# Kernel optimization log

Measured on AMD Instinct MI355X. Metric: run time of the kernel, lower is better.

The kernel has to match this reference:

```python
import jax, jax.numpy as jnp
import numpy as np

DIM = 1024
NUM_HEADS = 16
HEAD_DIM = DIM // NUM_HEADS
SCALE = HEAD_DIM ** -0.5


def setup_inputs() -> dict:
    key = jax.random.key(0)
    k_x, k_wqkv, k_bqkv, k_wp, k_bp = jax.random.split(key, 5)
    B, C, D = 4, 1024, DIM
    x = jax.random.normal(k_x, (B, C, D), dtype=jnp.float32)
    # nn.Linear stores weight as (out, in); we keep (in, out) for x @ W
    w_qkv = jax.random.normal(k_wqkv, (D, 3 * D), dtype=jnp.float32) * (D ** -0.5)
    b_qkv = jax.random.normal(k_bqkv, (3 * D,), dtype=jnp.float32) * 0.02
    w_proj = jax.random.normal(k_wp, (D, D), dtype=jnp.float32) * (D ** -0.5)
    b_proj = jax.random.normal(k_bp, (D,), dtype=jnp.float32) * 0.02
    return {"x": x, "w_qkv": w_qkv, "b_qkv": b_qkv, "w_proj": w_proj, "b_proj": b_proj}


def reference(x, w_qkv, b_qkv, w_proj, b_proj):
    B, C, D = x.shape
    H, Hd = NUM_HEADS, HEAD_DIM
    qkv = x @ w_qkv + b_qkv                       # (B, C, 3D)
    qkv = qkv.reshape(B, C, 3, H, Hd)
    q = qkv[:, :, 0].transpose(0, 2, 1, 3)        # (B, H, C, Hd)
    k = qkv[:, :, 1].transpose(0, 2, 1, 3)
    v = qkv[:, :, 2].transpose(0, 2, 1, 3)
    attn = jnp.einsum('bhqd,bhkd->bhqk', q, k) * SCALE
    attn = jax.nn.softmax(attn, axis=-1)
    out = jnp.einsum('bhqk,bhkd->bhqd', attn, v)  # (B, H, C, Hd)
    out = out.transpose(0, 2, 1, 3).reshape(B, C, D)
    return out @ w_proj + b_proj
```

## Files before the change

kernel.cpp:

```cpp
#include <hip/hip_runtime.h>
#include <cstdint>

#define BB 4
#define CC 1024
#define DD 1024
#define HH 16
#define HD 64
#define NH3 3072

typedef __attribute__((ext_vector_type(8))) short short8;
typedef __attribute__((ext_vector_type(4))) float f32x4;

#define MFMA16(a, b, c) __builtin_amdgcn_mfma_f32_16x16x32_bf16(a, b, c, 0, 0, 0)

__device__ __forceinline__ void glds16(const void* g, void* l) {
    __builtin_amdgcn_global_load_lds(
        (const __attribute__((address_space(1))) void*)g,
        (__attribute__((address_space(3))) void*)l, 16, 0, 0);
}

__device__ __forceinline__ ushort f2bf(float f) {
    union { float f; uint32_t u; } v; v.f = f;
    uint32_t r = v.u + 0x7FFF + ((v.u >> 16) & 1);
    return (ushort)(r >> 16);
}

__device__ __forceinline__ uint32_t pack2bf(float a, float b) {
    return (uint32_t)f2bf(a) | ((uint32_t)f2bf(b) << 16);
}

__global__ __launch_bounds__(256)
void convert_f32_bf16(const float* __restrict__ in, ushort* __restrict__ out, int n4)
{
    int i = blockIdx.x * 256 + threadIdx.x;
    if (i < n4) {
        float4 v = ((const float4*)in)[i];
        ushort4 o;
        o.x = f2bf(v.x); o.y = f2bf(v.y); o.z = f2bf(v.z); o.w = f2bf(v.w);
        ((ushort4*)out)[i] = o;
    }
}

__global__ __launch_bounds__(256)
void transpose_w(const float* __restrict__ in, ushort* __restrict__ out, int K, int N)
{
    __shared__ float Ts[64 * 65];
    const int n0 = blockIdx.x * 64, k0 = blockIdx.y * 64;
    const int t = threadIdx.x;
    #pragma unroll
    for (int i = 0; i < 16; ++i) {
        int idx = t + i * 256;
        int r = idx >> 6, c = idx & 63;
        Ts[r * 65 + c] = in[(size_t)(k0 + r) * N + n0 + c];
    }
    __syncthreads();
    #pragma unroll
    for (int i = 0; i < 16; ++i) {
        int idx = t + i * 256;
        int rr = idx >> 6, cc = idx & 63;
        out[(size_t)(n0 + rr) * K + k0 + cc] = f2bf(Ts[cc * 65 + rr]);
    }
}

__global__ __launch_bounds__(256)
void vtrans(const ushort* __restrict__ vb, ushort* __restrict__ vt)
{
    __shared__ ushort Ts[64 * 66];
    const int ct = blockIdx.x, bh = blockIdx.y;
    const ushort* src = vb + ((size_t)bh * CC + ct * 64) * HD;
    ushort* dst = vt + (size_t)bh * HD * CC + ct * 64;
    const int t = threadIdx.x;
    #pragma unroll
    for (int i = 0; i < 16; ++i) {
        int idx = t + i * 256;
        int r = idx >> 6, c = idx & 63;
        Ts[r * 66 + c] = src[r * 64 + c];
    }
    __syncthreads();
    #pragma unroll
    for (int i = 0; i < 16; ++i) {
        int idx = t + i * 256;
        int hd = idx >> 6, c = idx & 63;
        dst[(size_t)hd * CC + c] = Ts[c * 66 + hd];
    }
}

template<int MODE>
__global__ __launch_bounds__(256)
void gemm_bt(const ushort* __restrict__ A, const ushort* __restrict__ Bt,
             const float* __restrict__ bias, float* __restrict__ Cf,
             ushort* __restrict__ qb, ushort* __restrict__ kb, ushort* __restrict__ vb,
             int M, int N, int K)
{
    __shared__ ushort As[128 * 32];
    __shared__ ushort Bs[128 * 32];

    const int tid = threadIdx.x;
    const int wid = tid >> 6, lane = tid & 63;
    const int quad = lane >> 4, l15 = lane & 15;
    const int m0 = blockIdx.y * 128, n0 = blockIdx.x * 128;
    const int wm = (wid >> 1) * 64, wn = (wid & 1) * 64;

    const int sr = lane >> 2;
    const int sc = lane & 3;

    f32x4 acc[4][4];
    #pragma unroll
    for (int i = 0; i < 4; ++i)
        #pragma unroll
        for (int j = 0; j < 4; ++j) acc[i][j] = (f32x4)(0.0f);

    for (int k0 = 0; k0 < K; k0 += 32) {
        __syncthreads();
        #pragma unroll
        for (int t = 0; t < 2; ++t) {
            int r = wid * 32 + t * 16 + sr;
            int cg = sc ^ ((r >> 1) & 3);
            glds16(A  + (size_t)(m0 + r) * K + k0 + cg * 8, As + (wid * 32 + t * 16) * 32);
            glds16(Bt + (size_t)(n0 + r) * K + k0 + cg * 8, Bs + (wid * 32 + t * 16) * 32);
        }
        __syncthreads();

        short8 af[4], bf[4];
        #pragma unroll
        for (int i = 0; i < 4; ++i) {
            int row = wm + i * 16 + l15;
            af[i] = *(const short8*)(As + row * 32 + (quad ^ ((row >> 1) & 3)) * 8);
            int col = wn + i * 16 + l15;
            bf[i] = *(const short8*)(Bs + col * 32 + (quad ^ ((col >> 1) & 3)) * 8);
        }
        #pragma unroll
        for (int i = 0; i < 4; ++i)
            #pragma unroll
            for (int j = 0; j < 4; ++j)
                acc[i][j] = MFMA16(af[i], bf[j], acc[i][j]);
    }

    if (MODE == 0) {
        #pragma unroll
        for (int i = 0; i < 4; ++i) {
            int row = m0 + wm + i * 16 + quad * 4;
            #pragma unroll
            for (int j = 0; j < 4; ++j) {
                int col = n0 + wn + j * 16 + l15;
                float bv = bias[col];
                #pragma unroll
                for (int r = 0; r < 4; ++r)
                    Cf[(size_t)(row + r) * N + col] = acc[i][j][r] + bv;
            }
        }
    } else {
        #pragma unroll
        for (int j = 0; j < 4; ++j) {
            int n = n0 + wn + j * 16 + l15;
            int three = n >> 10;
            int h = (n >> 6) & 15;
            int hd = n & 63;
            ushort* base = (three == 0) ? qb : ((three == 1) ? kb : vb);
            float scale = (three == 0) ? 0.1803368801f : 1.0f;
            float bv = bias[n];
            #pragma unroll
            for (int i = 0; i < 4; ++i) {
                int row = m0 + wm + i * 16 + quad * 4;
                #pragma unroll
                for (int r = 0; r < 4; ++r) {
                    int m = row + r;
                    int b = m >> 10, c = m & 1023;
                    base[((size_t)((b * HH + h) * CC) + c) * HD + hd] =
                        f2bf((acc[i][j][r] + bv) * scale);
                }
            }
        }
    }
}

__global__ __launch_bounds__(256)
void attn_mfma2(const ushort* __restrict__ qb, const ushort* __restrict__ kb,
                const ushort* __restrict__ vt, ushort* __restrict__ attnb)
{
    __shared__ ushort Qs[128 * 64];
    __shared__ ushort Ks[64 * 64];
    __shared__ ushort Vs[64 * 64];
    __shared__ ushort Ps[128 * 72];

    const int tid = threadIdx.x;
    const int wid = tid >> 6, lane = tid & 63;
    const int quad = lane >> 4, l15 = lane & 15;
    const int qt = blockIdx.x, bh = blockIdx.y;
    const int q0 = qt * 128;
    const int b = bh >> 4, h = bh & 15;

    const ushort* Qp  = qb + ((size_t)bh * CC + q0) * HD;
    const ushort* Kp  = kb + (size_t)bh * CC * HD;
    const ushort* Vtp = vt + (size_t)bh * HD * CC;

    const int sr = lane >> 3;
    const int sc = lane & 7;

    #pragma unroll
    for (int t = 0; t < 4; ++t) {
        int r = wid * 32 + t * 8 + sr;
        int cg = sc ^ (r & 7);
        glds16(Qp + (size_t)r * HD + cg * 8, Qs + (wid * 32 + t * 8) * 64);
    }
    __syncthreads();

    short8 qf[2][2];
    #pragma unroll
    for (int q2 = 0; q2 < 2; ++q2) {
        int row = wid * 32 + q2 * 16 + l15;
        #pragma unroll
        for (int s = 0; s < 2; ++s)
            qf[q2][s] = *(const short8*)(Qs + row * 64 + (((s * 4 + quad) ^ (row & 7)) * 8));
    }

    f32x4 oacc[2][4];
    #pragma unroll
    for (int q2 = 0; q2 < 2; ++q2)
        #pragma unroll
        for (int hb = 0; hb < 4; ++hb) oacc[q2][hb] = (f32x4)(0.0f);
    float lsum[2] = {0.0f, 0.0f};

    for (int kt = 0; kt < 16; ++kt) {
        __syncthreads();
        #pragma unroll
        for (int t = 0; t < 2; ++t) {
            int r = wid * 16 + t * 8 + sr;
            int cg = sc ^ (r & 7);
            glds16(Kp  + ((size_t)(kt * 64 + r)) * HD + cg * 8, Ks + (wid * 16 + t * 8) * 64);
            glds16(Vtp + (size_t)r * CC + kt * 64 + cg * 8,     Vs + (wid * 16 + t * 8) * 64);
        }
        __syncthreads();

        #pragma unroll
        for (int kb2 = 0; kb2 < 4; ++kb2) {
            int krow = kb2 * 16 + l15;
            short8 kf0 = *(const short8*)(Ks + krow * 64 + ((quad ^ (krow & 7)) * 8));
            short8 kf1 = *(const short8*)(Ks + krow * 64 + (((4 + quad) ^ (krow & 7)) * 8));
            #pragma unroll
            for (int q2 = 0; q2 < 2; ++q2) {
                f32x4 st = (f32x4)(0.0f);
                st = MFMA16(kf0, qf[q2][0], st);
                st = MFMA16(kf1, qf[q2][1], st);
                float p0 = exp2f(st[0]);
                float p1 = exp2f(st[1]);
                float p2 = exp2f(st[2]);
                float p3 = exp2f(st[3]);
                lsum[q2] += (p0 + p1) + (p2 + p3);
                int row = wid * 32 + q2 * 16 + l15;
                *(uint2*)(Ps + row * 72 + kb2 * 16 + quad * 4) =
                    make_uint2(pack2bf(p0, p1), pack2bf(p2, p3));
            }
        }

        short8 vf[4][2];
        #pragma unroll
        for (int hb = 0; hb < 4; ++hb) {
            int hr = hb * 16 + l15;
            vf[hb][0] = *(const short8*)(Vs + hr * 64 + ((quad ^ (hr & 7)) * 8));
            vf[hb][1] = *(const short8*)(Vs + hr * 64 + (((4 + quad) ^ (hr & 7)) * 8));
        }
        #pragma unroll
        for (int q2 = 0; q2 < 2; ++q2) {
            int row = wid * 32 + q2 * 16 + l15;
            short8 pf0 = *(const short8*)(Ps + row * 72 + quad * 8);
            short8 pf1 = *(const short8*)(Ps + row * 72 + 32 + quad * 8);
            #pragma unroll
            for (int hb = 0; hb < 4; ++hb) {
                oacc[q2][hb] = MFMA16(pf0, vf[hb][0], oacc[q2][hb]);
                oacc[q2][hb] = MFMA16(pf1, vf[hb][1], oacc[q2][hb]);
            }
        }
    }

    #pragma unroll
    for (int q2 = 0; q2 < 2; ++q2) {
        lsum[q2] += __shfl_xor(lsum[q2], 16);
        lsum[q2] += __shfl_xor(lsum[q2], 32);
    }

    #pragma unroll
    for (int q2 = 0; q2 < 2; ++q2) {
        #pragma unroll
        for (int r = 0; r < 4; ++r) {
            float inv = 1.0f / __shfl(lsum[q2], (lane & 48) | (quad * 4 + r));
            int c = q0 + wid * 32 + q2 * 16 + quad * 4 + r;
            #pragma unroll
            for (int hb = 0; hb < 4; ++hb) {
                int d = h * 64 + hb * 16 + l15;
                attnb[((size_t)(b * CC + c)) * DD + d] = f2bf(oacc[q2][hb][r] * inv);
            }
        }
    }
}

extern "C" void kernel_launch(void* const* d_in, const int* in_sizes, int n_in,
                              void* d_out, int out_size, void* d_ws, size_t ws_size,
                              hipStream_t stream)
{
    (void)in_sizes; (void)n_in; (void)out_size; (void)ws_size;
    const float* x      = (const float*)d_in[0];
    const float* w_qkv  = (const float*)d_in[1];
    const float* b_qkv  = (const float*)d_in[2];
    const float* w_proj = (const float*)d_in[3];
    const float* b_proj = (const float*)d_in[4];
    float* out = (float*)d_out;

    ushort* p = (ushort*)d_ws;
    ushort* xbf   = p;  p += (size_t)4 * 1024 * 1024;
    ushort* wqkvT = p;  p += (size_t)3 * 1024 * 1024;
    ushort* wprjT = p;  p += (size_t)1 * 1024 * 1024;
    ushort* qbuf  = p;  p += (size_t)4 * 1024 * 1024;
    ushort* kbuf  = p;  p += (size_t)4 * 1024 * 1024;
    ushort* vbuf  = p;  p += (size_t)4 * 1024 * 1024;
    ushort* vtb   = p;  p += (size_t)4 * 1024 * 1024;
    ushort* attnb = p;  p += (size_t)4 * 1024 * 1024;

    convert_f32_bf16<<<4096, 256, 0, stream>>>(x, xbf, 1024 * 1024);
    transpose_w<<<dim3(48, 16), 256, 0, stream>>>(w_qkv, wqkvT, DD, NH3);
    transpose_w<<<dim3(16, 16), 256, 0, stream>>>(w_proj, wprjT, DD, DD);

    gemm_bt<1><<<dim3(NH3 / 128, (BB * CC) / 128), 256, 0, stream>>>(
        xbf, wqkvT, b_qkv, nullptr, qbuf, kbuf, vbuf, BB * CC, NH3, DD);

    vtrans<<<dim3(16, 64), 256, 0, stream>>>(vbuf, vtb);

    attn_mfma2<<<dim3(8, 64), 256, 0, stream>>>(qbuf, kbuf, vtb, attnb);

    gemm_bt<0><<<dim3(DD / 128, (BB * CC) / 128), 256, 0, stream>>>(
        attnb, wprjT, b_proj, out, nullptr, nullptr, nullptr, BB * CC, DD, DD);
}
```

Baseline: 208.0 us.

## Double-buffer GEMM and attention tiles, fuse prep kernels, write V transposed

```diff
diff --git a/kernel.cpp b/kernel.cpp
--- a/kernel.cpp
+++ b/kernel.cpp
@@ -30,23 +30,33 @@
 }
 
 __global__ __launch_bounds__(256)
-void convert_f32_bf16(const float* __restrict__ in, ushort* __restrict__ out, int n4)
+void prep_kernel(const float* __restrict__ x, ushort* __restrict__ xbf,
+                 const float* __restrict__ wqkv, ushort* __restrict__ wqkvT,
+                 const float* __restrict__ wprj, ushort* __restrict__ wprjT)
 {
-    int i = blockIdx.x * 256 + threadIdx.x;
-    if (i < n4) {
-        float4 v = ((const float4*)in)[i];
+    __shared__ float Ts[64 * 65];
+    const int blk = blockIdx.x;
+    const int t = threadIdx.x;
+
+    if (blk < 4096) {
+        int i = blk * 256 + t;
+        float4 v = ((const float4*)x)[i];
         ushort4 o;
         o.x = f2bf(v.x); o.y = f2bf(v.y); o.z = f2bf(v.z); o.w = f2bf(v.w);
-        ((ushort4*)out)[i] = o;
-    }
-}
-
-__global__ __launch_bounds__(256)
-void transpose_w(const float* __restrict__ in, ushort* __restrict__ out, int K, int N)
-{
-    __shared__ float Ts[64 * 65];
-    const int n0 = blockIdx.x * 64, k0 = blockIdx.y * 64;
-    const int t = threadIdx.x;
+        ((ushort4*)xbf)[i] = o;
+        return;
+    }
+
+    const float* in; ushort* outp; int K, N, n0, k0;
+    if (blk < 4864) {
+        int bx = blk - 4096;
+        in = wqkv; outp = wqkvT; K = DD; N = NH3;
+        n0 = (bx % 48) * 64; k0 = (bx / 48) * 64;
+    } else {
+        int bx = blk - 4864;
+        in = wprj; outp = wprjT; K = DD; N = DD;
+        n0 = (bx % 16) * 64; k0 = (bx / 16) * 64;
+    }
     #pragma unroll
     for (int i = 0; i < 16; ++i) {
         int idx = t + i * 256;
@@ -58,30 +68,7 @@
     for (int i = 0; i < 16; ++i) {
         int idx = t + i * 256;
         int rr = idx >> 6, cc = idx & 63;
-        out[(size_t)(n0 + rr) * K + k0 + cc] = f2bf(Ts[cc * 65 + rr]);
-    }
-}
-
-__global__ __launch_bounds__(256)
-void vtrans(const ushort* __restrict__ vb, ushort* __restrict__ vt)
-{
-    __shared__ ushort Ts[64 * 66];
-    const int ct = blockIdx.x, bh = blockIdx.y;
-    const ushort* src = vb + ((size_t)bh * CC + ct * 64) * HD;
-    ushort* dst = vt + (size_t)bh * HD * CC + ct * 64;
-    const int t = threadIdx.x;
-    #pragma unroll
-    for (int i = 0; i < 16; ++i) {
-        int idx = t + i * 256;
-        int r = idx >> 6, c = idx & 63;
-        Ts[r * 66 + c] = src[r * 64 + c];
-    }
-    __syncthreads();
-    #pragma unroll
-    for (int i = 0; i < 16; ++i) {
-        int idx = t + i * 256;
-        int hd = idx >> 6, c = idx & 63;
-        dst[(size_t)hd * CC + c] = Ts[c * 66 + hd];
+        outp[(size_t)(n0 + rr) * K + k0 + cc] = f2bf(Ts[cc * 65 + rr]);
     }
 }
 
@@ -89,11 +76,11 @@
 __global__ __launch_bounds__(256)
 void gemm_bt(const ushort* __restrict__ A, const ushort* __restrict__ Bt,
              const float* __restrict__ bias, float* __restrict__ Cf,
-             ushort* __restrict__ qb, ushort* __restrict__ kb, ushort* __restrict__ vb,
+             ushort* __restrict__ qb, ushort* __restrict__ kb, ushort* __restrict__ vtb,
              int M, int N, int K)
 {
-    __shared__ ushort As[128 * 32];
-    __shared__ ushort Bs[128 * 32];
+    __shared__ ushort As[2][128 * 32];
+    __shared__ ushort Bs[2][128 * 32];
 
     const int tid = threadIdx.x;
     const int wid = tid >> 6, lane = tid & 63;
@@ -104,36 +91,52 @@
     const int sr = lane >> 2;
     const int sc = lane & 3;
 
+    const int r0 = wid * 32 + sr;
+    const int cg0 = sc ^ ((r0 >> 1) & 3);
+    const int cg1 = sc ^ (((r0 + 16) >> 1) & 3);
+    const ushort* Ar0 = A  + (size_t)(m0 + r0) * K + cg0 * 8;
+    const ushort* Ar1 = A  + (size_t)(m0 + r0 + 16) * K + cg1 * 8;
+    const ushort* Br0 = Bt + (size_t)(n0 + r0) * K + cg0 * 8;
+    const ushort* Br1 = Bt + (size_t)(n0 + r0 + 16) * K + cg1 * 8;
+
     f32x4 acc[4][4];
     #pragma unroll
     for (int i = 0; i < 4; ++i)
         #pragma unroll
         for (int j = 0; j < 4; ++j) acc[i][j] = (f32x4)(0.0f);
 
+    {
+        glds16(Ar0, &As[0][(wid * 32) * 32]);
+        glds16(Br0, &Bs[0][(wid * 32) * 32]);
+        glds16(Ar1, &As[0][(wid * 32 + 16) * 32]);
+        glds16(Br1, &Bs[0][(wid * 32 + 16) * 32]);
+    }
+
+    int buf = 0;
     for (int k0 = 0; k0 < K; k0 += 32) {
         __syncthreads();
-        #pragma unroll
-        for (int t = 0; t < 2; ++t) {
-            int r = wid * 32 + t * 16 + sr;
-            int cg = sc ^ ((r >> 1) & 3);
-            glds16(A  + (size_t)(m0 + r) * K + k0 + cg * 8, As + (wid * 32 + t * 16) * 32);
-            glds16(Bt + (size_t)(n0 + r) * K + k0 + cg * 8, Bs + (wid * 32 + t * 16) * 32);
-        }
-        __syncthreads();
+        if (k0 + 32 < K) {
+            const int kn = k0 + 32;
+            glds16(Ar0 + kn, &As[buf ^ 1][(wid * 32) * 32]);
+            glds16(Br0 + kn, &Bs[buf ^ 1][(wid * 32) * 32]);
+            glds16(Ar1 + kn, &As[buf ^ 1][(wid * 32 + 16) * 32]);
+            glds16(Br1 + kn, &Bs[buf ^ 1][(wid * 32 + 16) * 32]);
+        }
 
         short8 af[4], bf[4];
         #pragma unroll
         for (int i = 0; i < 4; ++i) {
             int row = wm + i * 16 + l15;
-            af[i] = *(const short8*)(As + row * 32 + (quad ^ ((row >> 1) & 3)) * 8);
+            af[i] = *(const short8*)(&As[buf][row * 32 + (quad ^ ((row >> 1) & 3)) * 8]);
             int col = wn + i * 16 + l15;
-            bf[i] = *(const short8*)(Bs + col * 32 + (quad ^ ((col >> 1) & 3)) * 8);
+            bf[i] = *(const short8*)(&Bs[buf][col * 32 + (quad ^ ((col >> 1) & 3)) * 8]);
         }
         #pragma unroll
         for (int i = 0; i < 4; ++i)
             #pragma unroll
             for (int j = 0; j < 4; ++j)
                 acc[i][j] = MFMA16(af[i], bf[j], acc[i][j]);
+        buf ^= 1;
     }
 
     if (MODE == 0) {
@@ -156,7 +159,6 @@
             int three = n >> 10;
             int h = (n >> 6) & 15;
             int hd = n & 63;
-            ushort* base = (three == 0) ? qb : ((three == 1) ? kb : vb);
             float scale = (three == 0) ? 0.1803368801f : 1.0f;
             float bv = bias[n];
             #pragma unroll
@@ -166,8 +168,13 @@
                 for (int r = 0; r < 4; ++r) {
                     int m = row + r;
                     int b = m >> 10, c = m & 1023;
-                    base[((size_t)((b * HH + h) * CC) + c) * HD + hd] =
-                        f2bf((acc[i][j][r] + bv) * scale);
+                    ushort val = f2bf((acc[i][j][r] + bv) * scale);
+                    if (three == 0)
+                        qb[((size_t)((b * HH + h) * CC) + c) * HD + hd] = val;
+                    else if (three == 1)
+                        kb[((size_t)((b * HH + h) * CC) + c) * HD + hd] = val;
+                    else
+                        vtb[((size_t)((b * HH + h) * HD) + hd) * CC + c] = val;
                 }
             }
         }
@@ -175,12 +182,11 @@
 }
 
 __global__ __launch_bounds__(256)
-void attn_mfma2(const ushort* __restrict__ qb, const ushort* __restrict__ kb,
+void attn_mfma3(const ushort* __restrict__ qb, const ushort* __restrict__ kb,
                 const ushort* __restrict__ vt, ushort* __restrict__ attnb)
 {
-    __shared__ ushort Qs[128 * 64];
-    __shared__ ushort Ks[64 * 64];
-    __shared__ ushort Vs[64 * 64];
+    __shared__ ushort Ks[2][64 * 64];
+    __shared__ ushort Vs[2][64 * 64];
     __shared__ ushort Ps[128 * 72];
 
     const int tid = threadIdx.x;
@@ -197,22 +203,27 @@
     const int sr = lane >> 3;
     const int sc = lane & 7;
 
-    #pragma unroll
-    for (int t = 0; t < 4; ++t) {
-        int r = wid * 32 + t * 8 + sr;
-        int cg = sc ^ (r & 7);
-        glds16(Qp + (size_t)r * HD + cg * 8, Qs + (wid * 32 + t * 8) * 64);
-    }
-    __syncthreads();
-
     short8 qf[2][2];
     #pragma unroll
     for (int q2 = 0; q2 < 2; ++q2) {
         int row = wid * 32 + q2 * 16 + l15;
         #pragma unroll
         for (int s = 0; s < 2; ++s)
-            qf[q2][s] = *(const short8*)(Qs + row * 64 + (((s * 4 + quad) ^ (row & 7)) * 8));
-    }
+            qf[q2][s] = *(const short8*)(Qp + (size_t)row * HD + (s * 4 + quad) * 8);
+    }
+
+    const int kr = wid * 16 + sr;
+    const int cgA = sc ^ (kr & 7);
+    const int cgB = sc ^ ((kr + 8) & 7);
+    const ushort* Kr0 = Kp  + (size_t)kr * HD + cgA * 8;
+    const ushort* Kr1 = Kp  + (size_t)(kr + 8) * HD + cgB * 8;
+    const ushort* Vr0 = Vtp + (size_t)kr * CC + cgA * 8;
+    const ushort* Vr1 = Vtp + (size_t)(kr + 8) * CC + cgB * 8;
+
+    glds16(Kr0, &Ks[0][(wid * 16) * 64]);
+    glds16(Vr0, &Vs[0][(wid * 16) * 64]);
+    glds16(Kr1, &Ks[0][(wid * 16 + 8) * 64]);
+    glds16(Vr1, &Vs[0][(wid * 16 + 8) * 64]);
 
     f32x4 oacc[2][4];
     #pragma unroll
@@ -221,22 +232,22 @@
         for (int hb = 0; hb < 4; ++hb) oacc[q2][hb] = (f32x4)(0.0f);
     float lsum[2] = {0.0f, 0.0f};
 
+    int buf = 0;
     for (int kt = 0; kt < 16; ++kt) {
         __syncthreads();
-        #pragma unroll
-        for (int t = 0; t < 2; ++t) {
-            int r = wid * 16 + t * 8 + sr;
-            int cg = sc ^ (r & 7);
-            glds16(Kp  + ((size_t)(kt * 64 + r)) * HD + cg * 8, Ks + (wid * 16 + t * 8) * 64);
-            glds16(Vtp + (size_t)r * CC + kt * 64 + cg * 8,     Vs + (wid * 16 + t * 8) * 64);
-        }
-        __syncthreads();
+        if (kt < 15) {
+            const int koff = (kt + 1) * 64;
+            glds16(Kr0 + (size_t)koff * HD, &Ks[buf ^ 1][(wid * 16) * 64]);
+            glds16(Vr0 + koff,              &Vs[buf ^ 1][(wid * 16) * 64]);
+            glds16(Kr1 + (size_t)koff * HD, &Ks[buf ^ 1][(wid * 16 + 8) * 64]);
+            glds16(Vr1 + koff,              &Vs[buf ^ 1][(wid * 16 + 8) * 64]);
+        }
 
         #pragma unroll
         for (int kb2 = 0; kb2 < 4; ++kb2) {
             int krow = kb2 * 16 + l15;
-            short8 kf0 = *(const short8*)(Ks + krow * 64 + ((quad ^ (krow & 7)) * 8));
-            short8 kf1 = *(const short8*)(Ks + krow * 64 + (((4 + quad) ^ (krow & 7)) * 8));
+            short8 kf0 = *(const short8*)(&Ks[buf][krow * 64 + ((quad ^ (krow & 7)) * 8)]);
+            short8 kf1 = *(const short8*)(&Ks[buf][krow * 64 + (((4 + quad) ^ (krow & 7)) * 8)]);
             #pragma unroll
             for (int q2 = 0; q2 < 2; ++q2) {
                 f32x4 st = (f32x4)(0.0f);
@@ -257,8 +268,8 @@
         #pragma unroll
         for (int hb = 0; hb < 4; ++hb) {
             int hr = hb * 16 + l15;
-            vf[hb][0] = *(const short8*)(Vs + hr * 64 + ((quad ^ (hr & 7)) * 8));
-            vf[hb][1] = *(const short8*)(Vs + hr * 64 + (((4 + quad) ^ (hr & 7)) * 8));
+            vf[hb][0] = *(const short8*)(&Vs[buf][hr * 64 + ((quad ^ (hr & 7)) * 8)]);
+            vf[hb][1] = *(const short8*)(&Vs[buf][hr * 64 + (((4 + quad) ^ (hr & 7)) * 8)]);
         }
         #pragma unroll
         for (int q2 = 0; q2 < 2; ++q2) {
@@ -271,6 +282,7 @@
                 oacc[q2][hb] = MFMA16(pf1, vf[hb][1], oacc[q2][hb]);
             }
         }
+        buf ^= 1;
     }
 
     #pragma unroll
@@ -312,20 +324,15 @@
     ushort* wprjT = p;  p += (size_t)1 * 1024 * 1024;
     ushort* qbuf  = p;  p += (size_t)4 * 1024 * 1024;
     ushort* kbuf  = p;  p += (size_t)4 * 1024 * 1024;
-    ushort* vbuf  = p;  p += (size_t)4 * 1024 * 1024;
     ushort* vtb   = p;  p += (size_t)4 * 1024 * 1024;
     ushort* attnb = p;  p += (size_t)4 * 1024 * 1024;
 
-    convert_f32_bf16<<<4096, 256, 0, stream>>>(x, xbf, 1024 * 1024);
-    transpose_w<<<dim3(48, 16), 256, 0, stream>>>(w_qkv, wqkvT, DD, NH3);
-    transpose_w<<<dim3(16, 16), 256, 0, stream>>>(w_proj, wprjT, DD, DD);
+    prep_kernel<<<5120, 256, 0, stream>>>(x, xbf, w_qkv, wqkvT, w_proj, wprjT);
 
     gemm_bt<1><<<dim3(NH3 / 128, (BB * CC) / 128), 256, 0, stream>>>(
-        xbf, wqkvT, b_qkv, nullptr, qbuf, kbuf, vbuf, BB * CC, NH3, DD);
-
-    vtrans<<<dim3(16, 64), 256, 0, stream>>>(vbuf, vtb);
-
-    attn_mfma2<<<dim3(8, 64), 256, 0, stream>>>(qbuf, kbuf, vtb, attnb);
+        xbf, wqkvT, b_qkv, nullptr, qbuf, kbuf, vtb, BB * CC, NH3, DD);
+
+    attn_mfma3<<<dim3(8, 64), 256, 0, stream>>>(qbuf, kbuf, vtb, attnb);
 
     gemm_bt<0><<<dim3(DD / 128, (BB * CC) / 128), 256, 0, stream>>>(
         attnb, wprjT, b_proj, out, nullptr, nullptr, nullptr, BB * CC, DD, DD);
```

Result: faster. 191.8 us (-7.8%).
